# Optimization experiments

Hardware: AMD Instinct MI355X
Metric: run time of the kernel (lower is better)

Reference implementation:

```python
import jax, jax.numpy as jnp
import numpy as np
import math

NN_K = 32          # num_neighbor = ceil(k/dilation) = 32
MAP_SIZE = 32
GROUP = 4


def _fibonacci_sphere(samples):
    # matches fibonacci_sphere(samples, randomize=False): rnd = 1.0
    pts = [[0.0, 0.0, 0.0]]
    offset = 2.0 / samples
    increment = math.pi * (3.0 - math.sqrt(5.0))
    for i in range(samples - 1):
        y = i * offset - 1 + offset / 2.0
        r = math.sqrt(1.0 - y * y)
        phi = ((i + 1.0) % samples) * increment
        pts.append([math.cos(phi) * r, y, math.sin(phi) * r])
    return np.asarray(pts, dtype=np.float32)


def setup_inputs() -> dict:
    B, N, C_in, C_out = 8, 2048, 64, 128
    key = jax.random.key(0)
    ks = jax.random.split(key, 6)
    x = jax.random.normal(ks[0], (B, 3, N), dtype=jnp.float32)
    feature = jax.random.normal(ks[1], (B, C_in, N), dtype=jnp.float32)
    neigh_indexs = jax.random.randint(ks[2], (B, N, NN_K), 0, N, dtype=jnp.int32)
    B_rff = jax.random.normal(ks[3], (7, MAP_SIZE), dtype=jnp.float32)  # frozen RFF proj
    kernels = jnp.asarray(_fibonacci_sphere(NN_K).T)                    # [3, NN_K], frozen
    mlp_w = jax.random.normal(ks[4], (C_in, 2 * MAP_SIZE), dtype=jnp.float32) * 0.05
    mlp_b = jnp.zeros((C_in,), dtype=jnp.float32)
    conv_w = jax.random.normal(ks[5], (C_out, 2 * C_in * NN_K), dtype=jnp.float32) * 0.02
    conv_b = jnp.zeros((C_out,), dtype=jnp.float32)
    return {"x": x, "feature": feature, "neigh_indexs": neigh_indexs,
            "B_rff": B_rff, "kernels": kernels,
            "mlp_w": mlp_w, "mlp_b": mlp_b, "conv_w": conv_w, "conv_b": conv_b}


def _topkmax(perm):
    # two normalization passes over axis=1 (rows), squaring in between, then hard threshold
    perm = perm / (jnp.sum(perm, axis=1, keepdims=True) + 1e-6)
    perm = perm * perm
    perm = perm / (jnp.sum(perm, axis=1, keepdims=True) + 1e-6)
    return jnp.where(perm > 0.1, perm, 0.0)


def _paiconv(x, feature, neigh_indexs, B_rff, kernels, mlp_w, mlp_b, conv_w, conv_b):
    bsz, C, N = feature.shape           # B, num_feat, num_pts
    nn_k = neigh_indexs.shape[-1]
    xp = jnp.transpose(x, (0, 2, 1))    # [B, N, 3]

    # neighbor gather of coordinates -> [B*N, nn, 3]
    x_neighs = jax.vmap(lambda p, i: p[i])(xp, neigh_indexs).reshape(bsz * N, nn_k, 3)
    x_rep = jnp.broadcast_to(x_neighs[:, :1, :], x_neighs.shape)
    x_rel = x_neighs - x_rep
    x_dis = jnp.linalg.norm(x_rel, axis=-1, keepdims=True)

    # random Fourier features + 1x1 conv (mlp)
    pos = (2.0 * math.pi) * jnp.concatenate([x_rep, x_rel, x_dis], axis=-1)  # [BN, nn, 7]
    xf = pos @ B_rff                                                          # [BN, nn, 32]
    xf = jnp.concatenate([jnp.sin(xf), jnp.cos(xf)], axis=-1)                 # [BN, nn, 64]
    xf = jnp.einsum('oc,bnc->bon', mlp_w, xf) + mlp_b[None, :, None]          # [BN, C, nn]

    # neighbor gather of features -> [BN, C, nn], concat with positional feats
    fp = jnp.transpose(feature, (0, 2, 1))                                    # [B, N, C]
    f_nb = jax.vmap(lambda p, i: p[i])(fp, neigh_indexs).reshape(bsz * N, nn_k, C)
    feats = jnp.concatenate([jnp.transpose(f_nb, (0, 2, 1)), xf], axis=1)     # [BN, 2C, nn]

    # permutation/attention matrix
    one_pad = jnp.zeros((nn_k, nn_k), dtype=x.dtype).at[0, 0].set(1.0)
    perm = x_rel @ kernels + one_pad                                          # [BN, nn, nn]
    perm = jnp.where(perm > 0, perm, 0.0)
    perm = _topkmax(perm)

    if C > 3:  # static channel shuffle with group=4
        feats = feats.reshape(bsz * N, GROUP, 2 * C // GROUP, nn_k)
        feats = jnp.transpose(feats, (0, 2, 1, 3)).reshape(bsz * N, 2 * C, nn_k)

    feats = feats @ perm                                                      # [BN, 2C, nn]
    feats = feats.reshape(bsz * N, 2 * C * nn_k)
    out = feats @ conv_w.T + conv_b                                           # [BN, out_c]
    return jnp.transpose(out.reshape(bsz, N, -1), (0, 2, 1))                  # [B, out_c, N]


def reference(x, feature, neigh_indexs, B_rff, kernels, mlp_w, mlp_b, conv_w, conv_b):
    return _paiconv(x, feature, neigh_indexs, B_rff, kernels, mlp_w, mlp_b, conv_w, conv_b)
```

## Files before the change

kernel.cpp:

```cpp
#include <hip/hip_runtime.h>
#include <hip/hip_bf16.h>

typedef unsigned short ushort_t;
typedef __attribute__((ext_vector_type(8))) short short8;
typedef __attribute__((ext_vector_type(4))) float floatx4;

#define TWO_PI 6.28318530717958647692f

__device__ __forceinline__ float bf2f(ushort_t u) {
  union { unsigned u; float f; } v; v.u = ((unsigned)u) << 16; return v.f;
}
__device__ __forceinline__ unsigned pk(float a, float b) {
  union { __hip_bfloat162 h2; unsigned u; } v;
  v.h2 = __float22bfloat162_rn(make_float2(a, b));
  return v.u;
}
__device__ __forceinline__ float ldin(const void* p, int idx, bool bf) {
  return bf ? bf2f(((const ushort_t*)p)[idx]) : ((const float*)p)[idx];
}
__device__ __forceinline__ bool detect_bf16(const void* xv) {
  const ushort_t* us = (const ushort_t*)xv;
  unsigned u = us[threadIdx.x & 63];
  int e = (u >> 7) & 0xFF;
  bool good = (e >= 110) && (e <= 133);
  unsigned long long m = __ballot(good);
  return __builtin_popcountll(m) >= 52;
}
__device__ __forceinline__ uint4 pack8f(const float* p) {
  float4 a = *(const float4*)p, b = *(const float4*)(p + 4);
  uint4 r;
  r.x = pk(a.x, a.y); r.y = pk(a.z, a.w);
  r.z = pk(b.x, b.y); r.w = pk(b.z, b.w);
  return r;
}

__global__ __launch_bounds__(256) void paiconv_prep(
    const void* __restrict__ xprobe, const void* __restrict__ feat,
    ushort_t* __restrict__ Ft, const void* __restrict__ W,
    ushort_t* __restrict__ Wc)
{
  const bool bfm = detect_bf16(xprobe);
  const int t = threadIdx.x;
  __shared__ ushort_t tile[64 * 72];

  if (blockIdx.x >= 256) {
    int i = ((blockIdx.x - 256) * 256 + t) << 3;
    int n = i >> 12, rem = i & 4095;
    int c = rem >> 5, j = rem & 31;
    int src = (n << 12) + (((c & 31) * 4 + (c >> 5)) << 5) + j;
    if (bfm) *(uint4*)(Wc + i) = *(const uint4*)((const ushort_t*)W + src);
    else     *(uint4*)(Wc + i) = pack8f((const float*)W + src);
    return;
  }

  const int bb = blockIdx.x >> 5;
  const int n0 = (blockIdx.x & 31) << 6;
  {
    const int c = t & 63, ng = t >> 6;
    size_t base = (((size_t)(bb * 64 + c)) << 11) + n0 + (ng << 4);
    ushort_t v[16];
    if (bfm) {
      const ushort_t* fp_ = (const ushort_t*)feat + base;
      uint4 a = *(const uint4*)fp_, b2 = *(const uint4*)(fp_ + 8);
      unsigned uu[8] = {a.x, a.y, a.z, a.w, b2.x, b2.y, b2.z, b2.w};
#pragma unroll
      for (int e = 0; e < 8; ++e) {
        v[2 * e] = (ushort_t)(uu[e] & 0xffff);
        v[2 * e + 1] = (ushort_t)(uu[e] >> 16);
      }
    } else {
      const float* fp_ = (const float*)feat + base;
#pragma unroll
      for (int k = 0; k < 16; k += 2) {
        unsigned u = pk(fp_[k], fp_[k + 1]);
        v[k] = (ushort_t)(u & 0xffff);
        v[k + 1] = (ushort_t)(u >> 16);
      }
    }
#pragma unroll
    for (int k = 0; k < 16; ++k) tile[(ng * 16 + k) * 72 + c] = v[k];
  }
  __syncthreads();
  {
    const int nn = t >> 2, qtr = t & 3;
    uint4 w0 = *(const uint4*)(tile + nn * 72 + qtr * 16);
    uint4 w1 = *(const uint4*)(tile + nn * 72 + qtr * 16 + 8);
    ushort_t* dst = Ft + (((size_t)(bb * 2048 + n0 + nn)) << 6) + (qtr << 4);
    *(uint4*)dst = w0;
    *(uint4*)(dst + 8) = w1;
  }
}

#define SFPT 5184
__global__ __launch_bounds__(256) void paiconv_phase1(
    const void* __restrict__ x,
    const ushort_t* __restrict__ Ft,
    const int*  __restrict__ nbr,
    const void* __restrict__ Brff,
    const void* __restrict__ kern,
    const void* __restrict__ mlpw,
    const void* __restrict__ mlpb,
    ushort_t*   __restrict__ Ag)
{
  const bool bfm = detect_bf16(x);
  const int t = threadIdx.x;
  const int p0 = blockIdx.x << 1;
  const int b  = p0 >> 11;
  const int w = t >> 6, lane = t & 63, lrow = lane & 15, quad = lane >> 4;

  __shared__ ushort_t sRt[64 * 72];
  __shared__ ushort_t sF[SFPT];
  __shared__ ushort_t sP[2 * 32 * 40];
  __shared__ float sRel[2][32][3];
  __shared__ float sDis[2][32];
  __shared__ float sRep[2][3];
  __shared__ float sBr[224];

  const int gpt = t >> 7, gj = (t >> 2) & 31, gch = t & 3;
  const int gidx = nbr[((p0 + gpt) << 5) + gj];
  const ushort_t* gfr = Ft + (((size_t)(b * 2048 + gidx)) << 6) + (gch << 4);
  uint4 g0 = ((const uint4*)gfr)[0];
  uint4 g1 = ((const uint4*)gfr)[1];

  const int pj = t & 31;
  const float kn0 = ldin(kern, pj, bfm);
  const float kn1 = ldin(kern, 32 + pj, bfm);
  const float kn2 = ldin(kern, 64 + pj, bfm);
  const int mc = (w << 4) + lrow;
  const float bv = ldin(mlpb, mc, bfm);

  short8 mb0, mb1;
  if (bfm) {
    const ushort_t* mp = (const ushort_t*)mlpw + mc * 64;
    mb0 = *(const short8*)(mp + (quad << 3));
    mb1 = *(const short8*)(mp + 32 + (quad << 3));
  } else {
    const float* mp = (const float*)mlpw + mc * 64;
    uint4 u0 = pack8f(mp + (quad << 3));
    uint4 u1 = pack8f(mp + 32 + (quad << 3));
    mb0 = *(short8*)&u0;
    mb1 = *(short8*)&u1;
  }

  if (t < 224) sBr[t] = ldin(Brff, t, bfm);
  if (t < 64) {
    int pt = t >> 5, i = t & 31;
    int p = p0 + pt;
    int idx  = nbr[(p << 5) + i];
    int idx0 = nbr[(p << 5)];
    int xo = b * 6144;
    float rx = ldin(x, xo + idx0, bfm);
    float ry = ldin(x, xo + 2048 + idx0, bfm);
    float rz = ldin(x, xo + 4096 + idx0, bfm);
    float cx = ldin(x, xo + idx, bfm);
    float cy = ldin(x, xo + 2048 + idx, bfm);
    float cz = ldin(x, xo + 4096 + idx, bfm);
    float dx = cx - rx, dy = cy - ry, dz = cz - rz;
    sRel[pt][i][0] = dx; sRel[pt][i][1] = dy; sRel[pt][i][2] = dz;
    sDis[pt][i] = sqrtf(dx * dx + dy * dy + dz * dz);
    if (i == 0) { sRep[pt][0] = rx; sRep[pt][1] = ry; sRep[pt][2] = rz; }
  }
  __syncthreads();

  {
    int jn = t >> 2, mh = (t & 3) << 3;
    int pt = jn >> 5, j = jn & 31;
    float pos[7];
    pos[0] = TWO_PI * sRep[pt][0]; pos[1] = TWO_PI * sRep[pt][1];
    pos[2] = TWO_PI * sRep[pt][2];
    pos[3] = TWO_PI * sRel[pt][j][0]; pos[4] = TWO_PI * sRel[pt][j][1];
    pos[5] = TWO_PI * sRel[pt][j][2];
    pos[6] = TWO_PI * sDis[pt][j];
    unsigned sw[4], cw[4];
#pragma unroll
    for (int mm = 0; mm < 8; mm += 2) {
      float a0 = 0.f, a1 = 0.f;
#pragma unroll
      for (int d = 0; d < 7; ++d) {
        a0 += pos[d] * sBr[d * 32 + mh + mm];
        a1 += pos[d] * sBr[d * 32 + mh + mm + 1];
      }
      sw[mm >> 1] = pk(__sinf(a0), __sinf(a1));
      cw[mm >> 1] = pk(__cosf(a0), __cosf(a1));
    }
    ushort_t* rb = sRt + jn * 72;
    *(uint4*)(rb + mh)      = make_uint4(sw[0], sw[1], sw[2], sw[3]);
    *(uint4*)(rb + 32 + mh) = make_uint4(cw[0], cw[1], cw[2], cw[3]);
  }
  if (t < 128) {
    int pt = t >> 6, h = (t >> 5) & 1;
    float col[16];
    float s1 = 0.f;
#pragma unroll
    for (int il = 0; il < 16; ++il) {
      int i = h * 16 + il;
      float v = sRel[pt][i][0] * kn0 + sRel[pt][i][1] * kn1 + sRel[pt][i][2] * kn2;
      if (i == 0 && pj == 0) v += 1.0f;
      v = fmaxf(v, 0.f);
      col[il] = v; s1 += v;
    }
    s1 += __shfl_xor(s1, 32, 64);
    float inv1 = 1.0f / (s1 + 1e-6f);
    float s2 = 0.f;
#pragma unroll
    for (int il = 0; il < 16; ++il) { float v = col[il] * inv1; v = v * v; col[il] = v; s2 += v; }
    s2 += __shfl_xor(s2, 32, 64);
    float inv2 = 1.0f / (s2 + 1e-6f);
    unsigned pw[8];
#pragma unroll
    for (int il = 0; il < 16; il += 2) {
      float v0 = col[il] * inv2;     v0 = (v0 > 0.1f) ? v0 : 0.f;
      float v1 = col[il + 1] * inv2; v1 = (v1 > 0.1f) ? v1 : 0.f;
      pw[il >> 1] = pk(v0, v1);
    }
    ushort_t* dst = sP + pt * 1280 + pj * 40 + h * 16;
    *(uint4*)dst       = make_uint4(pw[0], pw[1], pw[2], pw[3]);
    *(uint4*)(dst + 8) = make_uint4(pw[4], pw[5], pw[6], pw[7]);
  }
  __syncthreads();

  const int rbase = (64 + mc) * 40 + ((4 + w) << 3);

#pragma unroll
  for (int pt = 0; pt < 2; ++pt) {
    {
#pragma unroll
      for (int half = 0; half < 2; ++half) {
        int mt = pt * 2 + half;
        const ushort_t* rp = sRt + (mt * 16 + lrow) * 72 + (quad << 3);
        short8 a0 = *(const short8*)rp;
        short8 a1 = *(const short8*)(rp + 32);
        floatx4 acc = {0.f, 0.f, 0.f, 0.f};
        acc = __builtin_amdgcn_mfma_f32_16x16x32_bf16(a0, mb0, acc, 0, 0, 0);
        acc = __builtin_amdgcn_mfma_f32_16x16x32_bf16(a1, mb1, acc, 0, 0, 0);
        int j0 = (half << 4) + (quad << 2);
        *(uint2*)(sF + rbase + j0) =
            make_uint2(pk(acc[0] + bv, acc[1] + bv), pk(acc[2] + bv, acc[3] + bv));
      }
      if (gpt == pt) {
        ushort_t* fp_ = sF + gch * 648 + gj;
        unsigned uu[8] = {g0.x, g0.y, g0.z, g0.w, g1.x, g1.y, g1.z, g1.w};
#pragma unroll
        for (int u = 0; u < 8; ++u) {
          fp_[(2 * u) * 40]     = (ushort_t)(uu[u] & 0xffff);
          fp_[(2 * u + 1) * 40] = (ushort_t)(uu[u] >> 16);
        }
      }
    }
    __syncthreads();

    {
      const ushort_t* Pp = sP + pt * 1280;
      short8 a0 = *(const short8*)(Pp + lrow * 40 + (quad << 3));
      short8 a1 = *(const short8*)(Pp + (16 + lrow) * 40 + (quad << 3));
      size_t prow = ((size_t)(p0 + pt)) << 12;
#pragma unroll
      for (int nt = 0; nt < 2; ++nt) {
        int blk = w * 2 + nt;
        int cidx = (blk << 4) + lrow;
        short8 bfg = *(const short8*)(sF + cidx * 40 + (blk << 3) + (quad << 3));
        floatx4 z = {0.f, 0.f, 0.f, 0.f};
        floatx4 c0 = __builtin_amdgcn_mfma_f32_16x16x32_bf16(a0, bfg, z, 0, 0, 0);
        floatx4 c1 = __builtin_amdgcn_mfma_f32_16x16x32_bf16(a1, bfg, z, 0, 0, 0);
        ushort_t* ad = Ag + prow + cidx * 32 + (quad << 2);
        *(uint2*)ad        = make_uint2(pk(c0[0], c0[1]), pk(c0[2], c0[3]));
        *(uint2*)(ad + 16) = make_uint2(pk(c1[0], c1[1]), pk(c1[2], c1[3]));
      }
    }
    if (pt == 0) __syncthreads();
  }
}

__global__ __launch_bounds__(256) void paiconv_gemm(
    const ushort_t* __restrict__ A,
    const ushort_t* __restrict__ Wc,
    float* __restrict__ part)
{
  __shared__ ushort_t lA[2][64 * 72];
  __shared__ ushort_t lB[2][128 * 72];
  const int m0 = blockIdx.x << 6;
  const int K0 = blockIdx.y << 11;
  const int t = threadIdx.x;
  const int w = t >> 6, lane = t & 63;
  const int wm = w & 1, wn = w >> 1, lrow = lane & 15, quad = lane >> 4;

  const int ar = t >> 2, ac = (t & 3) << 4;
  const int wr = t >> 1, wc = (t & 1) << 5;
  const ushort_t* Ap = A + (size_t)(m0 + ar) * 4096 + K0 + ac;
  const ushort_t* Wp = Wc + (size_t)wr * 4096 + K0 + wc;

  uint4 ea0 = *(const uint4*)Ap,        ea1 = *(const uint4*)(Ap + 8);
  uint4 eb0 = *(const uint4*)Wp,        eb1 = *(const uint4*)(Wp + 8);
  uint4 eb2 = *(const uint4*)(Wp + 16), eb3 = *(const uint4*)(Wp + 24);
  uint4 oa0 = *(const uint4*)(Ap + 64),      oa1 = *(const uint4*)(Ap + 72);
  uint4 ob0 = *(const uint4*)(Wp + 64),      ob1 = *(const uint4*)(Wp + 72);
  uint4 ob2 = *(const uint4*)(Wp + 80),      ob3 = *(const uint4*)(Wp + 88);

  floatx4 acc[2][4];
#pragma unroll
  for (int i = 0; i < 2; ++i)
#pragma unroll
    for (int j = 0; j < 4; ++j) acc[i][j] = (floatx4){0.f, 0.f, 0.f, 0.f};

  for (int kb = 0; kb < 32; kb += 2) {
    {
      ushort_t* la = lA[0];
      ushort_t* lb = lB[0];
      *(uint4*)(la + ar * 72 + ac)      = ea0;
      *(uint4*)(la + ar * 72 + ac + 8)  = ea1;
      *(uint4*)(lb + wr * 72 + wc)      = eb0;
      *(uint4*)(lb + wr * 72 + wc + 8)  = eb1;
      *(uint4*)(lb + wr * 72 + wc + 16) = eb2;
      *(uint4*)(lb + wr * 72 + wc + 24) = eb3;
      __syncthreads();
      if (kb + 2 < 32) {
        int off = (kb + 2) << 6;
        ea0 = *(const uint4*)(Ap + off);      ea1 = *(const uint4*)(Ap + off + 8);
        eb0 = *(const uint4*)(Wp + off);      eb1 = *(const uint4*)(Wp + off + 8);
        eb2 = *(const uint4*)(Wp + off + 16); eb3 = *(const uint4*)(Wp + off + 24);
      }
#pragma unroll
      for (int kk = 0; kk < 2; ++kk) {
        short8 af0 = *(const short8*)(la + ((wm << 5) + lrow) * 72 + (kk << 5) + (quad << 3));
        short8 af1 = *(const short8*)(la + ((wm << 5) + 16 + lrow) * 72 + (kk << 5) + (quad << 3));
#pragma unroll
        for (int ni = 0; ni < 4; ++ni) {
          short8 bf = *(const short8*)(lb + ((wn << 6) + (ni << 4) + lrow) * 72 +
                                       (kk << 5) + (quad << 3));
          acc[0][ni] = __builtin_amdgcn_mfma_f32_16x16x32_bf16(af0, bf, acc[0][ni], 0, 0, 0);
          acc[1][ni] = __builtin_amdgcn_mfma_f32_16x16x32_bf16(af1, bf, acc[1][ni], 0, 0, 0);
        }
      }
    }
    {
      ushort_t* la = lA[1];
      ushort_t* lb = lB[1];
      *(uint4*)(la + ar * 72 + ac)      = oa0;
      *(uint4*)(la + ar * 72 + ac + 8)  = oa1;
      *(uint4*)(lb + wr * 72 + wc)      = ob0;
      *(uint4*)(lb + wr * 72 + wc + 8)  = ob1;
      *(uint4*)(lb + wr * 72 + wc + 16) = ob2;
      *(uint4*)(lb + wr * 72 + wc + 24) = ob3;
      __syncthreads();
      if (kb + 3 < 32) {
        int off = (kb + 3) << 6;
        oa0 = *(const uint4*)(Ap + off);      oa1 = *(const uint4*)(Ap + off + 8);
        ob0 = *(const uint4*)(Wp + off);      ob1 = *(const uint4*)(Wp + off + 8);
        ob2 = *(const uint4*)(Wp + off + 16); ob3 = *(const uint4*)(Wp + off + 24);
      }
#pragma unroll
      for (int kk = 0; kk < 2; ++kk) {
        short8 af0 = *(const short8*)(la + ((wm << 5) + lrow) * 72 + (kk << 5) + (quad << 3));
        short8 af1 = *(const short8*)(la + ((wm << 5) + 16 + lrow) * 72 + (kk << 5) + (quad << 3));
#pragma unroll
        for (int ni = 0; ni < 4; ++ni) {
          short8 bf = *(const short8*)(lb + ((wn << 6) + (ni << 4) + lrow) * 72 +
                                       (kk << 5) + (quad << 3));
          acc[0][ni] = __builtin_amdgcn_mfma_f32_16x16x32_bf16(af0, bf, acc[0][ni], 0, 0, 0);
          acc[1][ni] = __builtin_amdgcn_mfma_f32_16x16x32_bf16(af1, bf, acc[1][ni], 0, 0, 0);
        }
      }
    }
  }

  float* dst = part + ((size_t)blockIdx.y << 21);
#pragma unroll
  for (int mi = 0; mi < 2; ++mi)
#pragma unroll
    for (int ni = 0; ni < 4; ++ni)
#pragma unroll
      for (int r = 0; r < 4; ++r) {
        int m = m0 + (wm << 5) + (mi << 4) + (quad << 2) + r;
        int n = (wn << 6) + (ni << 4) + lrow;
        dst[(size_t)m * 128 + n] = acc[mi][ni][r];
      }
}

__global__ __launch_bounds__(256) void paiconv_reduce(
    const void* __restrict__ xprobe, const float* __restrict__ part,
    const void* __restrict__ bias, void* __restrict__ out)
{
  const bool bfm = detect_bf16(xprobe);
  __shared__ float buf[128 * 65];
  const int m0 = blockIdx.x << 6;
  const int b = m0 >> 11, n0 = m0 & 2047;
  const int t = threadIdx.x;

#pragma unroll
  for (int i = 0; i < 8; ++i) {
    int idx = (i * 256 + t) << 2;
    int mt = idx >> 7, c = idx & 127;
    size_t o = (size_t)(m0 + mt) * 128 + c;
    float4 v0 = *(const float4*)(part + o);
    float4 v1 = *(const float4*)(part + (1u << 21) + o);
    buf[(c + 0) * 65 + mt] = v0.x + v1.x + ldin(bias, c + 0, bfm);
    buf[(c + 1) * 65 + mt] = v0.y + v1.y + ldin(bias, c + 1, bfm);
    buf[(c + 2) * 65 + mt] = v0.z + v1.z + ldin(bias, c + 2, bfm);
    buf[(c + 3) * 65 + mt] = v0.w + v1.w + ldin(bias, c + 3, bfm);
  }
  __syncthreads();
#pragma unroll
  for (int i = 0; i < 8; ++i) {
    int idx = (i * 256 + t) << 2;
    int c = idx >> 6, nl = idx & 63;
    float v0 = buf[c * 65 + nl], v1 = buf[c * 65 + nl + 1];
    float v2 = buf[c * 65 + nl + 2], v3 = buf[c * 65 + nl + 3];
    size_t o = (size_t)b * 262144 + (size_t)c * 2048 + n0 + nl;
    if (bfm) *(uint2*)((ushort_t*)out + o) = make_uint2(pk(v0, v1), pk(v2, v3));
    else     *(float4*)((float*)out + o) = make_float4(v0, v1, v2, v3);
  }
}

extern "C" void kernel_launch(void* const* d_in, const int* in_sizes, int n_in,
                              void* d_out, int out_size, void* d_ws, size_t ws_size,
                              hipStream_t stream) {
  const void* x     = d_in[0];
  const void* feat  = d_in[1];
  const int*  nbr   = (const int*)d_in[2];
  const void* Brff  = d_in[3];
  const void* kern  = d_in[4];
  const void* mlpw  = d_in[5];
  const void* mlpb  = d_in[6];
  const void* convw = d_in[7];
  const void* convb = d_in[8];

  char* ws = (char*)d_ws;
  ushort_t* A   = (ushort_t*)ws;
  ushort_t* Wcv = (ushort_t*)(ws + (size_t)134217728);
  float*    prt = (float*)(ws + (size_t)135266304);
  ushort_t* Ft  = (ushort_t*)(ws + (size_t)152043520);

  paiconv_prep<<<512, 256, 0, stream>>>(x, feat, Ft, convw, Wcv);
  paiconv_phase1<<<8192, 256, 0, stream>>>(x, Ft, nbr, Brff, kern, mlpw, mlpb, A);
  paiconv_gemm<<<dim3(256, 2, 1), 256, 0, stream>>>(A, Wcv, prt);
  paiconv_reduce<<<256, 256, 0, stream>>>(x, prt, convb, d_out);
}
```

Measured before the change: 166.3 us.

## Fuse GEMM with bias/transpose epilogue and drop split-K partials

The GEMM changes from a 64-row tile with split-K=2 (256x2 blocks) to a 32-row tile over the full K=4096 (512 blocks). Bias add, transpose and output store now happen in the GEMM epilogue through shared memory, so the separate reduce kernel and its fp32 partial buffer go away. This removes a kernel launch and the write-then-read of about 16MB of partials. In exchange, each block runs a K loop twice as long, and the smaller M tile means B tiles are reused less, so the weights are loaded from cache more often.

```diff
diff --git a/kernel.cpp b/kernel.cpp
--- a/kernel.cpp
+++ b/kernel.cpp
@@ -272,60 +272,61 @@
 }
 
 __global__ __launch_bounds__(256) void paiconv_gemm(
+    const void* __restrict__ xprobe,
     const ushort_t* __restrict__ A,
     const ushort_t* __restrict__ Wc,
-    float* __restrict__ part)
+    const void* __restrict__ bias,
+    void* __restrict__ out)
 {
-  __shared__ ushort_t lA[2][64 * 72];
-  __shared__ ushort_t lB[2][128 * 72];
-  const int m0 = blockIdx.x << 6;
-  const int K0 = blockIdx.y << 11;
+  const bool bfm = detect_bf16(xprobe);
+  __shared__ ushort_t smem[23040];
+  ushort_t* lAb[2] = { smem, smem + 2304 };
+  ushort_t* lBb[2] = { smem + 4608, smem + 13824 };
+  const int m0 = blockIdx.x << 5;
   const int t = threadIdx.x;
-  const int w = t >> 6, lane = t & 63;
-  const int wm = w & 1, wn = w >> 1, lrow = lane & 15, quad = lane >> 4;
-
-  const int ar = t >> 2, ac = (t & 3) << 4;
-  const int wr = t >> 1, wc = (t & 1) << 5;
-  const ushort_t* Ap = A + (size_t)(m0 + ar) * 4096 + K0 + ac;
-  const ushort_t* Wp = Wc + (size_t)wr * 4096 + K0 + wc;
-
-  uint4 ea0 = *(const uint4*)Ap,        ea1 = *(const uint4*)(Ap + 8);
+  const int w = t >> 6, lane = t & 63, lrow = lane & 15, quad = lane >> 4;
+
+  const int ar = t >> 3, ac = (t & 7) << 3;
+  const int wr = t >> 1, wcl = (t & 1) << 5;
+  const ushort_t* Ap = A + (size_t)(m0 + ar) * 4096 + ac;
+  const ushort_t* Wp = Wc + (size_t)wr * 4096 + wcl;
+
+  uint4 ea0 = *(const uint4*)Ap;
   uint4 eb0 = *(const uint4*)Wp,        eb1 = *(const uint4*)(Wp + 8);
   uint4 eb2 = *(const uint4*)(Wp + 16), eb3 = *(const uint4*)(Wp + 24);
-  uint4 oa0 = *(const uint4*)(Ap + 64),      oa1 = *(const uint4*)(Ap + 72);
-  uint4 ob0 = *(const uint4*)(Wp + 64),      ob1 = *(const uint4*)(Wp + 72);
-  uint4 ob2 = *(const uint4*)(Wp + 80),      ob3 = *(const uint4*)(Wp + 88);
-
-  floatx4 acc[2][4];
+  uint4 oa0 = *(const uint4*)(Ap + 64);
+  uint4 ob0 = *(const uint4*)(Wp + 64), ob1 = *(const uint4*)(Wp + 72);
+  uint4 ob2 = *(const uint4*)(Wp + 80), ob3 = *(const uint4*)(Wp + 88);
+
+  floatx4 acc[2][2];
 #pragma unroll
   for (int i = 0; i < 2; ++i)
 #pragma unroll
-    for (int j = 0; j < 4; ++j) acc[i][j] = (floatx4){0.f, 0.f, 0.f, 0.f};
-
-  for (int kb = 0; kb < 32; kb += 2) {
+    for (int j = 0; j < 2; ++j) acc[i][j] = (floatx4){0.f, 0.f, 0.f, 0.f};
+
+  for (int kb = 0; kb < 64; kb += 2) {
     {
-      ushort_t* la = lA[0];
-      ushort_t* lb = lB[0];
-      *(uint4*)(la + ar * 72 + ac)      = ea0;
-      *(uint4*)(la + ar * 72 + ac + 8)  = ea1;
-      *(uint4*)(lb + wr * 72 + wc)      = eb0;
-      *(uint4*)(lb + wr * 72 + wc + 8)  = eb1;
-      *(uint4*)(lb + wr * 72 + wc + 16) = eb2;
-      *(uint4*)(lb + wr * 72 + wc + 24) = eb3;
+      ushort_t* la = lAb[0];
+      ushort_t* lb = lBb[0];
+      *(uint4*)(la + ar * 72 + ac)       = ea0;
+      *(uint4*)(lb + wr * 72 + wcl)      = eb0;
+      *(uint4*)(lb + wr * 72 + wcl + 8)  = eb1;
+      *(uint4*)(lb + wr * 72 + wcl + 16) = eb2;
+      *(uint4*)(lb + wr * 72 + wcl + 24) = eb3;
       __syncthreads();
-      if (kb + 2 < 32) {
+      if (kb + 2 < 64) {
         int off = (kb + 2) << 6;
-        ea0 = *(const uint4*)(Ap + off);      ea1 = *(const uint4*)(Ap + off + 8);
+        ea0 = *(const uint4*)(Ap + off);
         eb0 = *(const uint4*)(Wp + off);      eb1 = *(const uint4*)(Wp + off + 8);
         eb2 = *(const uint4*)(Wp + off + 16); eb3 = *(const uint4*)(Wp + off + 24);
       }
 #pragma unroll
       for (int kk = 0; kk < 2; ++kk) {
-        short8 af0 = *(const short8*)(la + ((wm << 5) + lrow) * 72 + (kk << 5) + (quad << 3));
-        short8 af1 = *(const short8*)(la + ((wm << 5) + 16 + lrow) * 72 + (kk << 5) + (quad << 3));
-#pragma unroll
-        for (int ni = 0; ni < 4; ++ni) {
-          short8 bf = *(const short8*)(lb + ((wn << 6) + (ni << 4) + lrow) * 72 +
+        short8 af0 = *(const short8*)(la + lrow * 72 + (kk << 5) + (quad << 3));
+        short8 af1 = *(const short8*)(la + (16 + lrow) * 72 + (kk << 5) + (quad << 3));
+#pragma unroll
+        for (int ni = 0; ni < 2; ++ni) {
+          short8 bf = *(const short8*)(lb + ((w << 5) + (ni << 4) + lrow) * 72 +
                                        (kk << 5) + (quad << 3));
           acc[0][ni] = __builtin_amdgcn_mfma_f32_16x16x32_bf16(af0, bf, acc[0][ni], 0, 0, 0);
           acc[1][ni] = __builtin_amdgcn_mfma_f32_16x16x32_bf16(af1, bf, acc[1][ni], 0, 0, 0);
@@ -333,28 +334,27 @@
       }
     }
     {
-      ushort_t* la = lA[1];
-      ushort_t* lb = lB[1];
-      *(uint4*)(la + ar * 72 + ac)      = oa0;
-      *(uint4*)(la + ar * 72 + ac + 8)  = oa1;
-      *(uint4*)(lb + wr * 72 + wc)      = ob0;
-      *(uint4*)(lb + wr * 72 + wc + 8)  = ob1;
-      *(uint4*)(lb + wr * 72 + wc + 16) = ob2;
-      *(uint4*)(lb + wr * 72 + wc + 24) = ob3;
+      ushort_t* la = lAb[1];
+      ushort_t* lb = lBb[1];
+      *(uint4*)(la + ar * 72 + ac)       = oa0;
+      *(uint4*)(lb + wr * 72 + wcl)      = ob0;
+      *(uint4*)(lb + wr * 72 + wcl + 8)  = ob1;
+      *(uint4*)(lb + wr * 72 + wcl + 16) = ob2;
+      *(uint4*)(lb + wr * 72 + wcl + 24) = ob3;
       __syncthreads();
-      if (kb + 3 < 32) {
+      if (kb + 3 < 64) {
         int off = (kb + 3) << 6;
-        oa0 = *(const uint4*)(Ap + off);      oa1 = *(const uint4*)(Ap + off + 8);
+        oa0 = *(const uint4*)(Ap + off);
         ob0 = *(const uint4*)(Wp + off);      ob1 = *(const uint4*)(Wp + off + 8);
         ob2 = *(const uint4*)(Wp + off + 16); ob3 = *(const uint4*)(Wp + off + 24);
       }
 #pragma unroll
       for (int kk = 0; kk < 2; ++kk) {
-        short8 af0 = *(const short8*)(la + ((wm << 5) + lrow) * 72 + (kk << 5) + (quad << 3));
-        short8 af1 = *(const short8*)(la + ((wm << 5) + 16 + lrow) * 72 + (kk << 5) + (quad << 3));
-#pragma unroll
-        for (int ni = 0; ni < 4; ++ni) {
-          short8 bf = *(const short8*)(lb + ((wn << 6) + (ni << 4) + lrow) * 72 +
+        short8 af0 = *(const short8*)(la + lrow * 72 + (kk << 5) + (quad << 3));
+        short8 af1 = *(const short8*)(la + (16 + lrow) * 72 + (kk << 5) + (quad << 3));
+#pragma unroll
+        for (int ni = 0; ni < 2; ++ni) {
+          short8 bf = *(const short8*)(lb + ((w << 5) + (ni << 4) + lrow) * 72 +
                                        (kk << 5) + (quad << 3));
           acc[0][ni] = __builtin_amdgcn_mfma_f32_16x16x32_bf16(af0, bf, acc[0][ni], 0, 0, 0);
           acc[1][ni] = __builtin_amdgcn_mfma_f32_16x16x32_bf16(af1, bf, acc[1][ni], 0, 0, 0);
@@ -363,51 +363,30 @@
     }
   }
 
-  float* dst = part + ((size_t)blockIdx.y << 21);
+  __syncthreads();
+  float* buf = (float*)smem;
+  const int b = m0 >> 11, n0 = m0 & 2047;
 #pragma unroll
   for (int mi = 0; mi < 2; ++mi)
 #pragma unroll
-    for (int ni = 0; ni < 4; ++ni)
+    for (int ni = 0; ni < 2; ++ni) {
+      int n = (w << 5) + (ni << 4) + lrow;
+      float bvv = ldin(bias, n, bfm);
 #pragma unroll
       for (int r = 0; r < 4; ++r) {
-        int m = m0 + (wm << 5) + (mi << 4) + (quad << 2) + r;
-        int n = (wn << 6) + (ni << 4) + lrow;
-        dst[(size_t)m * 128 + n] = acc[mi][ni][r];
-      }
-}
-
-__global__ __launch_bounds__(256) void paiconv_reduce(
-    const void* __restrict__ xprobe, const float* __restrict__ part,
-    const void* __restrict__ bias, void* __restrict__ out)
-{
-  const bool bfm = detect_bf16(xprobe);
-  __shared__ float buf[128 * 65];
-  const int m0 = blockIdx.x << 6;
-  const int b = m0 >> 11, n0 = m0 & 2047;
-  const int t = threadIdx.x;
-
+        int m = (mi << 4) + (quad << 2) + r;
+        buf[n * 33 + m] = acc[mi][ni][r] + bvv;
+      }
+    }
+  __syncthreads();
 #pragma unroll
   for (int i = 0; i < 8; ++i) {
-    int idx = (i * 256 + t) << 2;
-    int mt = idx >> 7, c = idx & 127;
-    size_t o = (size_t)(m0 + mt) * 128 + c;
-    float4 v0 = *(const float4*)(part + o);
-    float4 v1 = *(const float4*)(part + (1u << 21) + o);
-    buf[(c + 0) * 65 + mt] = v0.x + v1.x + ldin(bias, c + 0, bfm);
-    buf[(c + 1) * 65 + mt] = v0.y + v1.y + ldin(bias, c + 1, bfm);
-    buf[(c + 2) * 65 + mt] = v0.z + v1.z + ldin(bias, c + 2, bfm);
-    buf[(c + 3) * 65 + mt] = v0.w + v1.w + ldin(bias, c + 3, bfm);
-  }
-  __syncthreads();
-#pragma unroll
-  for (int i = 0; i < 8; ++i) {
-    int idx = (i * 256 + t) << 2;
-    int c = idx >> 6, nl = idx & 63;
-    float v0 = buf[c * 65 + nl], v1 = buf[c * 65 + nl + 1];
-    float v2 = buf[c * 65 + nl + 2], v3 = buf[c * 65 + nl + 3];
-    size_t o = (size_t)b * 262144 + (size_t)c * 2048 + n0 + nl;
-    if (bfm) *(uint2*)((ushort_t*)out + o) = make_uint2(pk(v0, v1), pk(v2, v3));
-    else     *(float4*)((float*)out + o) = make_float4(v0, v1, v2, v3);
+    int idx = (i << 8) + t;
+    int c = idx >> 4, m2 = (idx & 15) << 1;
+    float v0 = buf[c * 33 + m2], v1 = buf[c * 33 + m2 + 1];
+    size_t o = (size_t)b * 262144 + (size_t)c * 2048 + n0 + m2;
+    if (bfm) *(unsigned*)((ushort_t*)out + o) = pk(v0, v1);
+    else     *(float2*)((float*)out + o) = make_float2(v0, v1);
   }
 }
 
@@ -427,11 +406,9 @@
   char* ws = (char*)d_ws;
   ushort_t* A   = (ushort_t*)ws;
   ushort_t* Wcv = (ushort_t*)(ws + (size_t)134217728);
-  float*    prt = (float*)(ws + (size_t)135266304);
   ushort_t* Ft  = (ushort_t*)(ws + (size_t)152043520);
 
   paiconv_prep<<<512, 256, 0, stream>>>(x, feat, Ft, convw, Wcv);
   paiconv_phase1<<<8192, 256, 0, stream>>>(x, Ft, nbr, Brff, kern, mlpw, mlpb, A);
-  paiconv_gemm<<<dim3(256, 2, 1), 256, 0, stream>>>(A, Wcv, prt);
-  paiconv_reduce<<<256, 256, 0, stream>>>(x, prt, convb, d_out);
-}
+  paiconv_gemm<<<512, 256, 0, stream>>>(x, A, Wcv, convb, d_out);
+}
```

Measured after the change: 169.3 us. About the same (+1.8%).
